# Kernel optimization log

Measured on AMD Instinct MI355X. Metric: run time of the kernel, lower is better.

The kernel has to match this reference:

```python
import jax, jax.numpy as jnp
import numpy as np

B, T, C, H = 4, 4096, 2048, 128


def setup_inputs() -> dict:
    key = jax.random.key(0)
    ks = jax.random.split(key, 7)
    s = 0.02
    return {
        "x": jax.random.normal(ks[0], (B, T, C), dtype=jnp.float32),
        "Wk": jax.random.normal(ks[1], (C, H), dtype=jnp.float32) * s,
        "bk": jax.random.normal(ks[2], (H,), dtype=jnp.float32) * s,
        "Wq": jax.random.normal(ks[3], (C, H), dtype=jnp.float32) * s,
        "bq": jax.random.normal(ks[4], (H,), dtype=jnp.float32) * s,
        "Wv": jax.random.normal(ks[5], (C, H), dtype=jnp.float32) * s,
        "bv": jax.random.normal(ks[6], (H,), dtype=jnp.float32) * s,
    }


def reference(x, Wk, bk, Wq, bq, Wv, bv):
    # x: [B, T, C]
    Bq, Tq, Cq = x.shape
    k = x @ Wk + bk  # [B, T, H]
    q = x @ Wq + bq
    v = x @ Wv + bv
    # NOTE: original scales by C**-0.5 (input emb dim), faithfully reproduced.
    scale = jnp.asarray(Cq, x.dtype) ** -0.5
    wei = jnp.einsum("bth,bsh->bts", q, k) * scale  # [B, T, T]
    causal = jnp.tril(jnp.ones((Tq, Tq), dtype=bool))
    wei = jnp.where(causal, wei, -jnp.inf)
    wei = jax.nn.softmax(wei, axis=-1)
    # dropout omitted (inference/eval mode)
    return jnp.einsum("bts,bsh->bth", wei, v)  # [B, T, H]
```

## Files before the change

### kernel.cpp

```cpp
#include <hip/hip_runtime.h>
#include <hip/hip_bf16.h>
#include <stdint.h>

#define T_SEQ 4096
#define C_DIM 2048
#define H_DIM 128
#define NBATCH 4

typedef unsigned short u16;
typedef __attribute__((ext_vector_type(8))) __bf16 bf16x8;
typedef __attribute__((ext_vector_type(4))) float f32x4;
typedef __attribute__((ext_vector_type(8))) unsigned short u16x8;
typedef __attribute__((ext_vector_type(4))) unsigned short u16x4;

__device__ __forceinline__ u16 f2bf(float f) {
  union { float f; uint32_t i; } v; v.f = f;
  uint32_t r = v.i + 0x7FFFu + ((v.i >> 16) & 1u);
  return (u16)(r >> 16);
}
__device__ __forceinline__ float bf2f(u16 u) {
  union { uint32_t i; float f; } v; v.i = ((uint32_t)u) << 16;
  return v.f;
}

__device__ __forceinline__ void gload16(const void* g, void* l) {
  __builtin_amdgcn_global_load_lds(
      (__attribute__((address_space(1))) void*)(g),
      (__attribute__((address_space(3))) void*)(l), 16, 0, 0);
}

__device__ __forceinline__ f32x4 mfma_bf16(bf16x8 a, bf16x8 b, f32x4 c) {
  return __builtin_amdgcn_mfma_f32_16x16x32_bf16(a, b, c, 0, 0, 0);
}

template<int CTRL>
__device__ __forceinline__ float dpp_mov(float x) {
  return __int_as_float(__builtin_amdgcn_mov_dpp(__float_as_int(x), CTRL, 0xF, 0xF, true));
}
__device__ __forceinline__ float red16_max(float v) {
  v = fmaxf(v, dpp_mov<0x121>(v));
  v = fmaxf(v, dpp_mov<0x122>(v));
  v = fmaxf(v, dpp_mov<0x124>(v));
  v = fmaxf(v, dpp_mov<0x128>(v));
  return v;
}
__device__ __forceinline__ float red16_sum(float v) {
  v += dpp_mov<0x121>(v);
  v += dpp_mov<0x122>(v);
  v += dpp_mov<0x124>(v);
  v += dpp_mov<0x128>(v);
  return v;
}

__global__ __launch_bounds__(256) void transpose_w(
    const float* __restrict__ Wq, const float* __restrict__ Wk,
    const float* __restrict__ Wv, u16* __restrict__ Wt)
{
  __shared__ u16 Wl[64 * 72];
  const int bk = blockIdx.x;
  const int bn = blockIdx.y;
  const int p  = blockIdx.z;
  const float* W = (p == 0) ? Wq : (p == 1) ? Wk : Wv;
  const int t = threadIdx.x;

  for (int ps = 0; ps < 16; ++ps) {
    int e  = ps * 256 + t;
    int kk = e >> 6, nn = e & 63;
    Wl[kk * 72 + nn] = f2bf(W[(size_t)(bk * 64 + kk) * H_DIM + bn * 64 + nn]);
  }
  __syncthreads();
  for (int ps = 0; ps < 16; ++ps) {
    int o  = ps * 256 + t;
    int nl = o >> 6, kl = o & 63;
    int n  = bn * 64 + nl;
    int g  = kl >> 3, j = kl & 7;
    int ks = ((g ^ (n & 7)) << 3) | j;
    Wt[(size_t)p * (H_DIM * C_DIM) + (size_t)n * C_DIM + bk * 64 + kl] = Wl[ks * 72 + nl];
  }
}

__global__ __launch_bounds__(512, 1) void qkv_fused(
    const float* __restrict__ x, const u16* __restrict__ Wt,
    const float* __restrict__ bq, const float* __restrict__ bk, const float* __restrict__ bv,
    u16* __restrict__ qo, u16* __restrict__ ko, u16* __restrict__ vTo)
{
  __shared__ alignas(16) u16 SMEM[2][28672];

  const int tid  = threadIdx.x;
  const int w    = tid >> 6, lane = tid & 63;
  const int t16  = lane & 15, quad = lane >> 4;
  const int mh   = w >> 2;
  const int nq   = w & 3;
  const int rt   = blockIdx.x;

  f32x4 acc[2][6];
  for (int i = 0; i < 2; ++i)
    for (int j = 0; j < 6; ++j) acc[i][j] = f32x4{0.f, 0.f, 0.f, 0.f};

  const size_t rowBase = (size_t)rt * 64;
  const int arow = tid >> 3;
  const int ag   = tid & 7;
  const float* xrow = &x[(rowBase + arow) * C_DIM + ag * 8];

  float4 a0 = ((const float4*)(xrow))[0];
  float4 a1 = ((const float4*)(xrow))[1];
  {
    u16* As = SMEM[0];
    u16* Bs = SMEM[0] + 4096;
    for (int p = 0; p < 3; ++p) {
      const u16* Wp = Wt + (size_t)p * (H_DIM * C_DIM);
      for (int j = 0; j < 2; ++j) {
        int e8 = (((j << 3) + w) * 64 + lane) * 8;
        int rr = e8 >> 6, kk = e8 & 63;
        gload16(Wp + (size_t)rr * C_DIM + kk, &Bs[p * 8192 + e8]);
      }
    }
    u16x8 pk;
    pk[0] = f2bf(a0.x); pk[1] = f2bf(a0.y); pk[2] = f2bf(a0.z); pk[3] = f2bf(a0.w);
    pk[4] = f2bf(a1.x); pk[5] = f2bf(a1.y); pk[6] = f2bf(a1.z); pk[7] = f2bf(a1.w);
    *(u16x8*)&As[arow * 64 + ((ag ^ (arow & 7)) << 3)] = pk;
  }
  a0 = ((const float4*)(xrow + 64))[0];
  a1 = ((const float4*)(xrow + 64))[1];

  for (int it = 0; it < 32; ++it) {
    const int cur = it & 1, nxt = cur ^ 1;
    __syncthreads();

    if (it + 1 < 32) {
      const int k1 = (it + 1) * 64;
      u16* As = SMEM[nxt];
      u16* Bs = SMEM[nxt] + 4096;
      for (int p = 0; p < 3; ++p) {
        const u16* Wp = Wt + (size_t)p * (H_DIM * C_DIM);
        for (int j = 0; j < 2; ++j) {
          int e8 = (((j << 3) + w) * 64 + lane) * 8;
          int rr = e8 >> 6, kk = e8 & 63;
          gload16(Wp + (size_t)rr * C_DIM + k1 + kk, &Bs[p * 8192 + e8]);
        }
      }
      u16x8 pk;
      pk[0] = f2bf(a0.x); pk[1] = f2bf(a0.y); pk[2] = f2bf(a0.z); pk[3] = f2bf(a0.w);
      pk[4] = f2bf(a1.x); pk[5] = f2bf(a1.y); pk[6] = f2bf(a1.z); pk[7] = f2bf(a1.w);
      *(u16x8*)&As[arow * 64 + ((ag ^ (arow & 7)) << 3)] = pk;
      if (it + 2 < 32) {
        const float4* xp = (const float4*)(xrow + (it + 2) * 64);
        a0 = xp[0]; a1 = xp[1];
      }
    }

    u16* As = SMEM[cur];
    u16* Bs = SMEM[cur] + 4096;
    for (int ks = 0; ks < 2; ++ks) {
      bf16x8 af[2], bfr[6];
      for (int ra = 0; ra < 2; ++ra)
        af[ra] = *(const bf16x8*)&As[(mh * 32 + ra * 16 + t16) * 64 +
                                     (((ks * 4 + quad) ^ (t16 & 7)) << 3)];
      for (int c = 0; c < 6; ++c) {
        int col = nq * 96 + c * 16 + t16;
        int p = col >> 7, pc = col & 127;
        bfr[c] = *(const bf16x8*)&Bs[p * 8192 + pc * 64 +
                                     (((ks * 4 + quad) ^ (t16 & 7)) << 3)];
      }
      for (int ra = 0; ra < 2; ++ra)
        for (int c = 0; c < 6; ++c)
          acc[ra][c] = mfma_bf16(af[ra], bfr[c], acc[ra][c]);
    }
  }

  __syncthreads();
  u16* Oq = SMEM[0];
  u16* Ok = SMEM[0] + 8192;
  u16* Ov = SMEM[0] + 16384;

  for (int c = 0; c < 6; ++c) {
    int col = nq * 96 + c * 16 + t16;
    int p = col >> 7, pc = col & 127;
    float bias = (p == 0) ? bq[pc] : (p == 1) ? bk[pc] : bv[pc];
    for (int ra = 0; ra < 2; ++ra) {
      for (int r = 0; r < 4; ++r) {
        int row16 = mh * 32 + ra * 16 + quad * 4 + r;
        float v = acc[ra][c][r] + bias;
        if (p == 2) {
          int gt = row16 >> 3;
          Ov[pc * 64 + ((gt ^ (pc & 7)) << 3) + (row16 & 7)] = f2bf(v);
        } else {
          u16* O = (p == 0) ? Oq : Ok;
          int g = pc >> 3;
          O[row16 * 128 + (((g ^ (row16 & 15)) << 3) | (pc & 7))] = f2bf(v);
        }
      }
    }
  }
  __syncthreads();

  const int bb = rt >> 6;
  const int tb = (rt & 63) * 64;
  for (int ps = 0; ps < 2; ++ps) {
    int c = ps * 512 + tid;
    {
      int row16 = c >> 4, g = c & 15;
      u16x8 v = *(const u16x8*)&Oq[row16 * 128 + ((g ^ (row16 & 15)) << 3)];
      *(u16x8*)&qo[(rowBase + row16) * H_DIM + g * 8] = v;
    }
    *(u16x8*)&ko[rowBase * H_DIM + c * 8] = *(const u16x8*)&Ok[c * 8];
    {
      int d = c >> 3, gc = c & 7;
      *(u16x8*)&vTo[((size_t)bb * H_DIM + d) * T_SEQ + tb + gc * 8] =
          *(const u16x8*)&Ov[c * 8];
    }
  }
}

__global__ __launch_bounds__(256, 2) void flash_attn(
    const u16* __restrict__ q, const u16* __restrict__ k,
    const u16* __restrict__ vT, float* __restrict__ out,
    void* __restrict__ OpartRaw, float* __restrict__ MLpart,
    int split, int pf32)
{
  __shared__ alignas(16) u16 Kt[2][64 * 128];
  __shared__ alignas(16) u16 Vt[2][128 * 64];
  __shared__ alignas(16) u16 Ps[4 * 16 * 72];

  const int tid  = threadIdx.x;
  const int w    = tid >> 6, lane = tid & 63;
  const int t16  = lane & 15, quad = lane >> 4;
  const int b    = blockIdx.x;

  int qt, kt0, ktn, mls, esd;
  if (split) {
    const int j = blockIdx.y;
    int c, n;
    if (j < 64)       { qt = 63 - (j >> 2); c = j & 3; n = 4; }
    else if (j < 112) { int t = j - 64; int d3 = t / 3; qt = 47 - d3; c = t - d3 * 3; n = 3; }
    else if (j < 144) { int t = j - 112; qt = 31 - (t >> 1); c = t & 1; n = 2; }
    else              { qt = 159 - j; c = 0; n = 1; }
    const int NT = qt + 1;
    kt0 = c * NT / n;
    ktn = (c + 1) * NT / n - kt0;
    if (n == 1) { mls = -1; esd = -1; }
    else {
      int mlb, esb;
      if (qt >= 48)      { mlb = (qt - 48) * 4;       esb = (qt - 48) * 3; }
      else if (qt >= 32) { mlb = 64 + (qt - 32) * 3;  esb = 48 + (qt - 32) * 2; }
      else               { mlb = 112 + (qt - 16) * 2; esb = 80 + (qt - 16); }
      mls = b * 144 + mlb + c;
      esd = (c >= 1) ? (b * 96 + esb + c - 1) : -2;
    }
  } else {
    qt = 63 - blockIdx.y; kt0 = 0; ktn = qt + 1; mls = -1; esd = -1;
  }

  const float SCALE = 0.022097086912079612f;
  const float L2E   = 1.4426950408889634f;

  bf16x8 qf[4];
  {
    const u16* qrow = q + ((size_t)(b * T_SEQ + qt * 64 + w * 16 + t16)) * H_DIM;
    for (int c = 0; c < 4; ++c)
      qf[c] = *(const bf16x8*)(qrow + c * 32 + quad * 8);
  }

  f32x4 Oc[8];
  for (int i = 0; i < 8; ++i) Oc[i] = f32x4{0.f, 0.f, 0.f, 0.f};
  float mrow[4] = {-1e30f, -1e30f, -1e30f, -1e30f};
  float lrow[4] = {0.f, 0.f, 0.f, 0.f};

  const u16* kbase = k  + ((size_t)b * T_SEQ) * H_DIM;
  const u16* vbase = vT + ((size_t)b * H_DIM) * T_SEQ;

  {
    const u16* kg = kbase + (size_t)(kt0 * 64) * H_DIM;
    for (int j = 0; j < 4; ++j) {
      int e8 = (((j << 2) + w) * 64 + lane) * 8;
      gload16(kg + e8, &Kt[0][e8]);
      int d = e8 >> 6, kk = e8 & 63;
      gload16(vbase + (size_t)d * T_SEQ + kt0 * 64 + kk, &Vt[0][e8]);
    }
  }

  int cur = 0;
  for (int it = 0; it < ktn; ++it) {
    const int kt = kt0 + it;
    __syncthreads();
    if (it + 1 < ktn) {
      const int nb = cur ^ 1, kt1 = kt + 1;
      const u16* kg = kbase + (size_t)(kt1 * 64) * H_DIM;
      for (int j = 0; j < 4; ++j) {
        int e8 = (((j << 2) + w) * 64 + lane) * 8;
        gload16(kg + e8, &Kt[nb][e8]);
        int d = e8 >> 6, kk = e8 & 63;
        gload16(vbase + (size_t)d * T_SEQ + kt1 * 64 + kk, &Vt[nb][e8]);
      }
    }

    f32x4 S[4];
    for (int ct = 0; ct < 4; ++ct) S[ct] = f32x4{0.f, 0.f, 0.f, 0.f};
    __builtin_amdgcn_s_setprio(1);
    for (int c = 0; c < 4; ++c) {
      for (int ct = 0; ct < 4; ++ct) {
        bf16x8 kf = *(const bf16x8*)&Kt[cur][(ct * 16 + t16) * H_DIM +
                                            (((c * 4 + quad) ^ t16) << 3)];
        S[ct] = mfma_bf16(qf[c], kf, S[ct]);
      }
    }
    __builtin_amdgcn_s_setprio(0);

    const bool diag = (kt == qt);
    for (int ct = 0; ct < 4; ++ct)
      for (int r = 0; r < 4; ++r) {
        float s = S[ct][r] * SCALE;
        if (diag && (ct * 16 + t16 > w * 16 + quad * 4 + r)) s = -1e30f;
        S[ct][r] = s;
      }

    float alpha[4], mnew[4];
    for (int r = 0; r < 4; ++r) {
      float mx = red16_max(fmaxf(fmaxf(S[0][r], S[1][r]), fmaxf(S[2][r], S[3][r])));
      mnew[r]  = fmaxf(mrow[r], mx);
      alpha[r] = exp2f((mrow[r] - mnew[r]) * L2E);
      mrow[r]  = mnew[r];
    }
    for (int r = 0; r < 4; ++r) {
      float s = 0.f;
      for (int ct = 0; ct < 4; ++ct) {
        float pv = exp2f((S[ct][r] - mnew[r]) * L2E);
        S[ct][r] = pv;
        s += pv;
      }
      lrow[r] = lrow[r] * alpha[r] + red16_sum(s);
    }
    for (int dt = 0; dt < 8; ++dt)
      for (int r = 0; r < 4; ++r)
        Oc[dt][r] *= alpha[r];

    u16* pw = &Ps[w * 1152];
    for (int ct = 0; ct < 4; ++ct)
      for (int r = 0; r < 4; ++r)
        pw[(quad * 4 + r) * 72 + ct * 16 + t16] = f2bf(S[ct][r]);
    __asm__ volatile("s_waitcnt lgkmcnt(0)" ::: "memory");

    __builtin_amdgcn_s_setprio(1);
    for (int ks = 0; ks < 2; ++ks) {
      bf16x8 pf = *(const bf16x8*)&pw[t16 * 72 + ks * 32 + quad * 8];
      for (int dt = 0; dt < 8; ++dt) {
        bf16x8 vf = *(const bf16x8*)&Vt[cur][(dt * 16 + t16) * 64 +
                                            (((ks * 4 + quad) ^ (t16 & 7)) << 3)];
        Oc[dt] = mfma_bf16(pf, vf, Oc[dt]);
      }
    }
    __builtin_amdgcn_s_setprio(0);
    cur ^= 1;
  }

  if (mls < 0) {
    for (int r = 0; r < 4; ++r) {
      float inv = 1.0f / lrow[r];
      size_t row = (size_t)b * T_SEQ + qt * 64 + w * 16 + quad * 4 + r;
      for (int dt = 0; dt < 8; ++dt)
        out[row * H_DIM + dt * 16 + t16] = Oc[dt][r] * inv;
    }
  } else {
    if (t16 == 0)
      for (int r = 0; r < 4; ++r) {
        int row = w * 16 + quad * 4 + r;
        MLpart[(size_t)mls * 128 + row * 2 + 0] = mrow[r];
        MLpart[(size_t)mls * 128 + row * 2 + 1] = lrow[r];
      }
    if (esd == -2) {
      for (int r = 0; r < 4; ++r) {
        size_t row = (size_t)b * T_SEQ + qt * 64 + w * 16 + quad * 4 + r;
        for (int dt = 0; dt < 8; ++dt)
          out[row * H_DIM + dt * 16 + t16] = Oc[dt][r];
      }
    } else if (pf32) {
      float* op = (float*)OpartRaw + (size_t)esd * 8192;
      for (int r = 0; r < 4; ++r) {
        int row = w * 16 + quad * 4 + r;
        for (int dt = 0; dt < 8; ++dt)
          op[row * 128 + dt * 16 + t16] = Oc[dt][r];
      }
    } else {
      u16* op = (u16*)OpartRaw + (size_t)esd * 8192;
      for (int r = 0; r < 4; ++r) {
        int row = w * 16 + quad * 4 + r;
        for (int dt = 0; dt < 8; ++dt)
          op[row * 128 + dt * 16 + t16] = f2bf(Oc[dt][r]);
      }
    }
  }
}

__global__ __launch_bounds__(256) void combine(
    const void* __restrict__ OpartRaw, const float* __restrict__ MLpart,
    float* __restrict__ out, int pf32)
{
  __shared__ float cs[4][64];
  const float L2E = 1.4426950408889634f;
  const int s = blockIdx.x;
  const int b = s / 48, qt = 16 + (s % 48);
  const int t = threadIdx.x;

  int n, mlb, esb;
  if (qt >= 48)      { n = 4; mlb = (qt - 48) * 4;       esb = (qt - 48) * 3; }
  else if (qt >= 32) { n = 3; mlb = 64 + (qt - 32) * 3;  esb = 48 + (qt - 32) * 2; }
  else               { n = 2; mlb = 112 + (qt - 16) * 2; esb = 80 + (qt - 16); }
  const int mls0 = b * 144 + mlb;
  const int esd0 = b * 96 + esb;

  if (t < 64) {
    float m[4], l[4];
    float mg = -1e30f;
    for (int c = 0; c < n; ++c) {
      const float* ML = MLpart + (size_t)(mls0 + c) * 128;
      m[c] = ML[t * 2]; l[c] = ML[t * 2 + 1];
      mg = fmaxf(mg, m[c]);
    }
    float denom = 0.f, e[4];
    for (int c = 0; c < n; ++c) {
      e[c] = exp2f((m[c] - mg) * L2E);
      denom += l[c] * e[c];
    }
    float inv = 1.0f / denom;
    for (int c = 0; c < n; ++c) cs[c][t] = e[c] * inv;
  }
  __syncthreads();

  float* o = out + ((size_t)b * T_SEQ + (size_t)qt * 64) * (size_t)H_DIM;
  for (int i4 = t; i4 < 2048; i4 += 256) {
    const int row = i4 >> 5;
    float4 acc = ((float4*)o)[i4];
    const float c0 = cs[0][row];
    acc.x *= c0; acc.y *= c0; acc.z *= c0; acc.w *= c0;
    for (int c = 1; c < n; ++c) {
      const float cc = cs[c][row];
      if (pf32) {
        const float4 p = ((const float4*)((const float*)OpartRaw +
                          (size_t)(esd0 + c - 1) * 8192))[i4];
        acc.x += p.x * cc; acc.y += p.y * cc;
        acc.z += p.z * cc; acc.w += p.w * cc;
      } else {
        const u16x4 p = ((const u16x4*)((const u16*)OpartRaw +
                         (size_t)(esd0 + c - 1) * 8192))[i4];
        acc.x += bf2f(p[0]) * cc; acc.y += bf2f(p[1]) * cc;
        acc.z += bf2f(p[2]) * cc; acc.w += bf2f(p[3]) * cc;
      }
    }
    ((float4*)o)[i4] = acc;
  }
}

extern "C" void kernel_launch(void* const* d_in, const int* in_sizes, int n_in,
                              void* d_out, int out_size, void* d_ws, size_t ws_size,
                              hipStream_t stream) {
  const float* x  = (const float*)d_in[0];
  const float* Wk = (const float*)d_in[1];
  const float* bk = (const float*)d_in[2];
  const float* Wq = (const float*)d_in[3];
  const float* bq = (const float*)d_in[4];
  const float* Wv = (const float*)d_in[5];
  const float* bv = (const float*)d_in[6];
  float* out = (float*)d_out;

  char* ws = (char*)d_ws;
  u16* qb  = (u16*)(ws);
  u16* kb  = (u16*)(ws + 4194304);
  u16* vT  = (u16*)(ws + 8388608);
  u16* Wt  = (u16*)(ws + 12582912);
  void* Opart = (void*)(ws + 14155776);

  const size_t base     = 14155776ull;
  const size_t ml_bytes = 294912ull;
  const size_t need_f32 = base + 12582912ull + ml_bytes;
  const size_t need_b16 = base + 6291456ull  + ml_bytes;

  int split, pf32;
  float* MLpart;
  if (ws_size >= need_f32) {
    split = 1; pf32 = 1;
    MLpart = (float*)(ws + base + 12582912ull);
  } else if (ws_size >= need_b16) {
    split = 1; pf32 = 0;
    MLpart = (float*)(ws + base + 6291456ull);
  } else {
    split = 0; pf32 = 0;
    MLpart = (float*)(ws + base);
  }

  hipLaunchKernelGGL(transpose_w, dim3(32, 2, 3), dim3(256), 0, stream, Wq, Wk, Wv, Wt);
  hipLaunchKernelGGL(qkv_fused, dim3(256), dim3(512), 0, stream,
                     x, Wt, bq, bk, bv, qb, kb, vT);
  hipLaunchKernelGGL(flash_attn, dim3(4, split ? 160 : 64), dim3(256), 0, stream,
                     qb, kb, vT, out, Opart, MLpart, split, pf32);
  if (split)
    hipLaunchKernelGGL(combine, dim3(192), dim3(256), 0, stream, Opart, MLpart, out, pf32);
}
```

Baseline: 299.1 us.

## Fold softmax scale into Q projection and use lazy max rescaling

Multiplies Q by the attention scale when the projection output is written, which removes the per-score scale multiply in the attention loop. The online softmax now updates the running max and rescales O and l only when a row's new max exceeds the old one by more than a threshold, and the rescale is skipped when no row needs it. This cuts VALU work on the inner loop. The cost is that scaled Q is rounded to bf16 after scaling, and exponent arguments can reach +8 before a rescale, which widens the range of the unnormalized values.

```diff
diff --git a/kernel.cpp b/kernel.cpp
--- a/kernel.cpp
+++ b/kernel.cpp
@@ -173,6 +173,7 @@
   u16* Ok = SMEM[0] + 8192;
   u16* Ov = SMEM[0] + 16384;
 
+  const float QSCALE = 0.022097086912079612f;
   for (int c = 0; c < 6; ++c) {
     int col = nq * 96 + c * 16 + t16;
     int p = col >> 7, pc = col & 127;
@@ -181,6 +182,7 @@
       for (int r = 0; r < 4; ++r) {
         int row16 = mh * 32 + ra * 16 + quad * 4 + r;
         float v = acc[ra][c][r] + bias;
+        if (p == 0) v *= QSCALE;
         if (p == 2) {
           int gt = row16 >> 3;
           Ov[pc * 64 + ((gt ^ (pc & 7)) << 3) + (row16 & 7)] = f2bf(v);
@@ -251,8 +253,7 @@
     qt = 63 - blockIdx.y; kt0 = 0; ktn = qt + 1; mls = -1; esd = -1;
   }
 
-  const float SCALE = 0.022097086912079612f;
-  const float L2E   = 1.4426950408889634f;
+  const float L2E = 1.4426950408889634f;
 
   bf16x8 qf[4];
   {
@@ -306,33 +307,39 @@
     }
     __builtin_amdgcn_s_setprio(0);
 
-    const bool diag = (kt == qt);
-    for (int ct = 0; ct < 4; ++ct)
-      for (int r = 0; r < 4; ++r) {
-        float s = S[ct][r] * SCALE;
-        if (diag && (ct * 16 + t16 > w * 16 + quad * 4 + r)) s = -1e30f;
-        S[ct][r] = s;
-      }
-
-    float alpha[4], mnew[4];
+    if (kt == qt) {
+      for (int ct = 0; ct < 4; ++ct)
+        for (int r = 0; r < 4; ++r)
+          if (ct * 16 + t16 > w * 16 + quad * 4 + r) S[ct][r] = -1e30f;
+    }
+
+    float alpha[4];
+    bool any = false;
     for (int r = 0; r < 4; ++r) {
       float mx = red16_max(fmaxf(fmaxf(S[0][r], S[1][r]), fmaxf(S[2][r], S[3][r])));
-      mnew[r]  = fmaxf(mrow[r], mx);
-      alpha[r] = exp2f((mrow[r] - mnew[r]) * L2E);
-      mrow[r]  = mnew[r];
+      if (mx > mrow[r] + 8.0f) {
+        alpha[r] = exp2f((mrow[r] - mx) * L2E);
+        mrow[r] = mx;
+        any = true;
+      } else {
+        alpha[r] = 1.0f;
+      }
+    }
+    if (any) {
+      for (int r = 0; r < 4; ++r) lrow[r] *= alpha[r];
+      for (int dt = 0; dt < 8; ++dt)
+        for (int r = 0; r < 4; ++r)
+          Oc[dt][r] *= alpha[r];
     }
     for (int r = 0; r < 4; ++r) {
       float s = 0.f;
       for (int ct = 0; ct < 4; ++ct) {
-        float pv = exp2f((S[ct][r] - mnew[r]) * L2E);
+        float pv = exp2f((S[ct][r] - mrow[r]) * L2E);
         S[ct][r] = pv;
         s += pv;
       }
-      lrow[r] = lrow[r] * alpha[r] + red16_sum(s);
-    }
-    for (int dt = 0; dt < 8; ++dt)
-      for (int r = 0; r < 4; ++r)
-        Oc[dt][r] *= alpha[r];
+      lrow[r] += red16_sum(s);
+    }
 
     u16* pw = &Ps[w * 1152];
     for (int ct = 0; ct < 4; ++ct)
```

Result: no change. 295.8 us (-1.1%).
